# Kernel optimization log

Measured on AMD Instinct MI355X. Metric: run time of the kernel, lower is better.

The kernel has to match this reference:

```python
import jax, jax.numpy as jnp
import numpy as np

H = 16       # num attention heads
DH = 128     # head dim
NEG = -1e9


def setup_inputs() -> dict:
    key = jax.random.key(0)
    ks = jax.random.split(key, 10)
    B, L, HID = 64, 4096, H * DH
    return {
        "hidden_states": jax.random.normal(ks[0], (B, HID), jnp.float32),
        "key_cache": jax.random.normal(ks[1], (B, L, DH), jnp.float32),
        "value_cache": jax.random.normal(ks[2], (B, L, DH), jnp.float32),
        "Wq": jax.random.normal(ks[3], (HID, HID), jnp.float32) * 0.02,
        "bq": jax.random.normal(ks[4], (HID,), jnp.float32) * 0.02,
        "Wkv": jax.random.normal(ks[5], (HID, 2 * DH), jnp.float32) * 0.02,
        "bkv": jax.random.normal(ks[6], (2 * DH,), jnp.float32) * 0.02,
        "Wo": jax.random.normal(ks[7], (HID, HID), jnp.float32) * 0.02,
        "bo": jax.random.normal(ks[8], (HID,), jnp.float32) * 0.02,
        "context_lens": jax.random.randint(ks[9], (B,), 0, L, jnp.int32),
    }


def reference(hidden_states, key_cache, value_cache, Wq, bq, Wkv, bkv, Wo, bo, context_lens):
    B, HID = hidden_states.shape
    L = key_cache.shape[1]
    scale = DH ** -0.5
    # QKV projections (MQA: single KV head)
    q = (hidden_states @ Wq + bq).reshape(B, H, DH)          # [B,H,Dh]
    kv = hidden_states @ Wkv + bkv                            # [B,2*Dh]
    k_new, v_new = kv[:, :DH], kv[:, DH:]                     # [B,Dh] each
    # Attention over paged KV cache (flattened per-sequence view) + current token
    s_cache = jnp.einsum('bhd,bld->bhl', q, key_cache) * scale   # [B,H,L]
    s_self = jnp.einsum('bhd,bd->bh', q, k_new) * scale          # [B,H]
    valid = (jnp.arange(L, dtype=jnp.int32)[None, None, :]
             < context_lens[:, None, None])                      # [B,1,L]
    s_cache = jnp.where(valid, s_cache, NEG)
    scores = jnp.concatenate([s_cache, s_self[..., None]], axis=-1)  # [B,H,L+1]
    p = jax.nn.softmax(scores, axis=-1)
    out = (jnp.einsum('bhl,bld->bhd', p[..., :L], value_cache)
           + p[..., L:] * v_new[:, None, :])                     # [B,H,Dh]
    return out.reshape(B, HID) @ Wo + bo
```

## Files before the change

kernel.cpp:

```cpp
#include <hip/hip_runtime.h>
#include <hip/hip_bf16.h>
#include <math.h>

#define H 16
#define DH 128
#define HID 2048
#define NB 64
#define LCACHE 4096
#define NS 16
#define NKS 16
#define SCALE 0.08838834764831845f

typedef __attribute__((ext_vector_type(8))) short bf16x8;
typedef __attribute__((ext_vector_type(4))) float f32x4;

static __device__ inline unsigned short bfr(float x) {
  union { __hip_bfloat16 b; unsigned short u; } c;
  c.b = __float2bfloat16(x);
  return c.u;
}
static __device__ inline unsigned pkbf(float lo, float hi) {
  return (unsigned)bfr(lo) | ((unsigned)bfr(hi) << 16);
}
union BFU { unsigned u[4]; bf16x8 v; };

__global__ __launch_bounds__(256) void transpose64(const float* __restrict__ A,
                                                   float* __restrict__ At) {
  __shared__ float tile[64 * 65];
  const int k0 = blockIdx.x * 64;
  for (int idx = threadIdx.x; idx < 4096; idx += 256) {
    const int m = idx >> 6, c = idx & 63;
    tile[c * 65 + m] = A[(size_t)m * HID + k0 + c];
  }
  __syncthreads();
  for (int idx = threadIdx.x; idx < 4096; idx += 256) {
    const int c = idx >> 6, m = idx & 63;
    At[(size_t)(k0 + c) * 64 + m] = tile[c * 65 + m];
  }
}

__global__ __launch_bounds__(256, 4) void proj_v2(
    const float* __restrict__ At, const float* __restrict__ W1, const float* __restrict__ W2,
    float* __restrict__ part, int NC1, int NC2) {
  const int NC = NC1 + NC2;
  const int n0 = blockIdx.x * 128;
  const int k0 = blockIdx.y * 128;
  __shared__ float Asub[128 * 68];
  const int t = threadIdx.x;
#pragma unroll
  for (int j = 0; j < 8; ++j) {
    const int f = t * 4 + j * 1024;
    const int k = f >> 6, m = f & 63;
    *(float4*)&Asub[k * 68 + m] = *(const float4*)(At + (size_t)(k0 + k) * 64 + m);
  }
  __syncthreads();
  const int m0 = (t & 15) * 4;
  const int ng = (t >> 4) * 8;
  const float* Wp;
  int ldw, wc;
  if (n0 + ng < NC1) { Wp = W1; ldw = NC1; wc = n0 + ng; }
  else               { Wp = W2; ldw = NC2; wc = n0 + ng - NC1; }
  float acc[4][8];
#pragma unroll
  for (int i = 0; i < 4; ++i)
#pragma unroll
    for (int j = 0; j < 8; ++j) acc[i][j] = 0.f;
#pragma unroll 4
  for (int k = 0; k < 128; ++k) {
    const float4 a4 = *(const float4*)&Asub[k * 68 + m0];
    const float* wrow = Wp + (size_t)(k0 + k) * ldw + wc;
    const float4 w0 = *(const float4*)(wrow);
    const float4 w1 = *(const float4*)(wrow + 4);
    const float av[4] = {a4.x, a4.y, a4.z, a4.w};
    const float wv[8] = {w0.x, w0.y, w0.z, w0.w, w1.x, w1.y, w1.z, w1.w};
#pragma unroll
    for (int i = 0; i < 4; ++i)
#pragma unroll
      for (int j = 0; j < 8; ++j) acc[i][j] = fmaf(av[i], wv[j], acc[i][j]);
  }
#pragma unroll
  for (int i = 0; i < 4; ++i) {
    float4 o1, o2;
    o1.x = acc[i][0]; o1.y = acc[i][1]; o1.z = acc[i][2]; o1.w = acc[i][3];
    o2.x = acc[i][4]; o2.y = acc[i][5]; o2.z = acc[i][6]; o2.w = acc[i][7];
    float* dst = part + ((size_t)blockIdx.y * 64 + m0 + i) * NC + n0 + ng;
    *(float4*)dst = o1;
    *(float4*)(dst + 4) = o2;
  }
}

__global__ __launch_bounds__(256) void proj_combine(
    const float* __restrict__ part, const float* __restrict__ b1, const float* __restrict__ b2,
    float* __restrict__ out1, float* __restrict__ out2, int NC1, int NC2) {
  const int NC = NC1 + NC2;
  const int f = (blockIdx.x * 256 + threadIdx.x) * 4;
  if (f >= 64 * NC) return;
  const int row = f / NC;
  const int c = f - row * NC;
  float4 s = *(const float4*)(part + (size_t)row * NC + c);
#pragma unroll
  for (int sp = 1; sp < NKS; ++sp) {
    const float4 p = *(const float4*)(part + ((size_t)sp * 64 + row) * NC + c);
    s.x += p.x; s.y += p.y; s.z += p.z; s.w += p.w;
  }
  if (c < NC1) {
    const float4 bb = *(const float4*)(b1 + c);
    s.x += bb.x; s.y += bb.y; s.z += bb.z; s.w += bb.w;
    *(float4*)(out1 + (size_t)row * NC1 + c) = s;
  } else {
    const int cc = c - NC1;
    const float4 bb = *(const float4*)(b2 + cc);
    s.x += bb.x; s.y += bb.y; s.z += bb.z; s.w += bb.w;
    *(float4*)(out2 + (size_t)row * NC2 + cc) = s;
  }
}

template <int NSPLIT>
__global__ __launch_bounds__(256, 3) void attn_mfma(
    const float* __restrict__ q_buf, const float* __restrict__ kv_buf,
    const float* __restrict__ key_cache, const float* __restrict__ value_cache,
    const int* __restrict__ lens,
    float* __restrict__ part_out, float* __restrict__ part_m, float* __restrict__ part_l) {
  const int b = blockIdx.y;
  const int sp = blockIdx.x;
  const int ctx = lens[b];
  const int n0 = (ctx * sp) / NSPLIT;
  const int n1 = (ctx * (sp + 1)) / NSPLIT;
  const int cnt = n1 - n0;
  const bool has_self = (sp == NSPLIT - 1);
  const int tot = cnt + (has_self ? 1 : 0);
  const int t = threadIdx.x;
  if (tot == 0) {
    if (t < H) {
      part_m[((size_t)b * NSPLIT + sp) * H + t] = -1e30f;
      part_l[((size_t)b * NSPLIT + sp) * H + t] = 0.f;
    }
    return;
  }
  __shared__ __align__(16) char regA[25024];
  __shared__ __align__(16) char regB[16384];
  __shared__ float red[16 * 17];
  __shared__ float mrow[16];
  __shared__ float selfp[16];

  float* q_s = (float*)regA;
  float* Sm = (float*)(regA + 8448);
  unsigned short* Vt = (unsigned short*)regA;
  char* Kl = regB;
  char* P = regB;

  for (int idx = t; idx < HID; idx += 256)
    q_s[(idx >> 7) * 132 + (idx & 127)] = q_buf[(size_t)b * HID + idx] * SCALE;

  const int lane = t & 63;
  const int wv = t >> 6;
  const int fh = lane & 15;
  const int fg = lane >> 4;
  const int si = t & 63;
  const int sc = t >> 6;
  const int vp = t & 31;
  const int vc = t >> 5;
  const int ntiles = (cnt + 63) >> 6;
  const float* ksrc = key_cache + (size_t)b * LCACHE * DH;
  const float* vsrc = value_cache + (size_t)b * LCACHE * DH;

  float4 kst[8];
  if (ntiles > 0) {
    const int r = min(n0 + si, LCACHE - 1);
    const float* src = ksrc + (size_t)r * DH + sc * 32;
#pragma unroll
    for (int j = 0; j < 8; ++j) kst[j] = *(const float4*)(src + j * 4);
  }
  __syncthreads();

  bf16x8 qf[4];
#pragma unroll
  for (int s = 0; s < 4; ++s) {
    const float4 qa = *(const float4*)&q_s[fh * 132 + s * 32 + fg * 8];
    const float4 qb = *(const float4*)&q_s[fh * 132 + s * 32 + fg * 8 + 4];
    BFU u;
    u.u[0] = pkbf(qa.x, qa.y); u.u[1] = pkbf(qa.z, qa.w);
    u.u[2] = pkbf(qb.x, qb.y); u.u[3] = pkbf(qb.z, qb.w);
    qf[s] = u.v;
  }

  for (int tt = 0; tt < ntiles; ++tt) {
    if (tt > 0) __syncthreads();
#pragma unroll
    for (int s2 = 0; s2 < 4; ++s2) {
      BFU u;
      u.u[0] = pkbf(kst[s2 * 2].x, kst[s2 * 2].y);
      u.u[1] = pkbf(kst[s2 * 2].z, kst[s2 * 2].w);
      u.u[2] = pkbf(kst[s2 * 2 + 1].x, kst[s2 * 2 + 1].y);
      u.u[3] = pkbf(kst[s2 * 2 + 1].z, kst[s2 * 2 + 1].w);
      const int off = si * 256 + ((sc * 64 + s2 * 16) ^ ((si & 7) << 4));
      *(bf16x8*)(Kl + off) = u.v;
    }
    if (tt + 1 < ntiles) {
      const int r = min(n0 + (tt + 1) * 64 + si, LCACHE - 1);
      const float* src = ksrc + (size_t)r * DH + sc * 32;
#pragma unroll
      for (int j = 0; j < 8; ++j) kst[j] = *(const float4*)(src + j * 4);
    }
    __syncthreads();
    f32x4 sacc = {0.f, 0.f, 0.f, 0.f};
    const int rr = wv * 16 + fh;
#pragma unroll
    for (int s = 0; s < 4; ++s) {
      const int off = rr * 256 + ((s * 64 + fg * 16) ^ ((rr & 7) << 4));
      const bf16x8 af = *(const bf16x8*)(Kl + off);
      sacc = __builtin_amdgcn_mfma_f32_16x16x32_bf16(af, qf[s], sacc, 0, 0, 0);
    }
    const int rowl = tt * 64 + wv * 16 + fg * 4;
#pragma unroll
    for (int j = 0; j < 4; ++j) {
      const int rw = rowl + j;
      if (rw < cnt) Sm[fh * 259 + rw] = sacc[j];
    }
  }

  if (ntiles > 0) {
    const int r0g = n0 + 2 * vp;
    const int ra = min(r0g, LCACHE - 1);
    const int rb = min(r0g + 1, LCACHE - 1);
    const float* sa = vsrc + (size_t)ra * DH + vc * 16;
    const float* sb = vsrc + (size_t)rb * DH + vc * 16;
#pragma unroll
    for (int j = 0; j < 4; ++j) {
      kst[j] = *(const float4*)(sa + j * 4);
      kst[4 + j] = *(const float4*)(sb + j * 4);
    }
  }

  if (has_self) {
    if (t < 128) {
      const int h = t >> 3;
      const int seg = t & 7;
      float ps = 0.f;
#pragma unroll
      for (int dd = 0; dd < 16; ++dd)
        ps += q_s[h * 132 + seg * 16 + dd] * kv_buf[(size_t)b * 256 + seg * 16 + dd];
      red[h * 8 + seg] = ps;
    }
    __syncthreads();
    if (t < H) {
      float s = 0.f;
#pragma unroll
      for (int seg = 0; seg < 8; ++seg) s += red[t * 8 + seg];
      Sm[t * 259 + cnt] = s;
    }
  }
  __syncthreads();

  const int hX = t & 15;
  const int g = t >> 4;
  float mloc = -1e30f;
  for (int i = g; i < tot; i += 16) mloc = fmaxf(mloc, Sm[hX * 259 + i]);
  red[hX * 17 + g] = mloc;
  __syncthreads();
  if (t < H) {
    float mx = red[t * 17];
#pragma unroll
    for (int gg = 1; gg < 16; ++gg) mx = fmaxf(mx, red[t * 17 + gg]);
    mrow[t] = mx;
  }
  __syncthreads();
  const float mh = mrow[hX];
  float sloc = 0.f;
  const int ipad = ntiles * 64;
  const int iend = (ipad > tot) ? ipad : tot;
  unsigned short* Pu = (unsigned short*)P;
  for (int i = g; i < iend; i += 16) {
    if (i < cnt) {
      const float e = __expf(Sm[hX * 259 + i] - mh);
      Pu[hX * 264 + i] = bfr(e);
      sloc += e;
    } else {
      if (i < ipad) Pu[hX * 264 + i] = 0;
      if (has_self && i == cnt) {
        const float e = __expf(Sm[hX * 259 + cnt] - mh);
        selfp[hX] = e;
        sloc += e;
      }
    }
  }
  red[hX * 17 + g] = sloc;
  __syncthreads();
  if (t < H) {
    float ls = 0.f;
#pragma unroll
    for (int gg = 0; gg < 16; ++gg) ls += red[t * 17 + gg];
    part_m[((size_t)b * NSPLIT + sp) * H + t] = mrow[t];
    part_l[((size_t)b * NSPLIT + sp) * H + t] = ls;
  }
  __syncthreads();

  f32x4 oacc[2];
  oacc[0] = (f32x4){0.f, 0.f, 0.f, 0.f};
  oacc[1] = (f32x4){0.f, 0.f, 0.f, 0.f};
  unsigned* VtW = (unsigned*)Vt;
  for (int tt = 0; tt < ntiles; ++tt) {
    if (tt > 0) __syncthreads();
#pragma unroll
    for (int j = 0; j < 4; ++j) {
      const float4 a = kst[j];
      const float4 b4 = kst[4 + j];
      const int d = vc * 16 + j * 4;
      VtW[(d + 0) * 44 + vp] = pkbf(a.x, b4.x);
      VtW[(d + 1) * 44 + vp] = pkbf(a.y, b4.y);
      VtW[(d + 2) * 44 + vp] = pkbf(a.z, b4.z);
      VtW[(d + 3) * 44 + vp] = pkbf(a.w, b4.w);
    }
    if (tt + 1 < ntiles) {
      const int r0g = n0 + (tt + 1) * 64 + 2 * vp;
      const int ra = min(r0g, LCACHE - 1);
      const int rb = min(r0g + 1, LCACHE - 1);
      const float* sa = vsrc + (size_t)ra * DH + vc * 16;
      const float* sb = vsrc + (size_t)rb * DH + vc * 16;
#pragma unroll
      for (int j = 0; j < 4; ++j) {
        kst[j] = *(const float4*)(sa + j * 4);
        kst[4 + j] = *(const float4*)(sb + j * 4);
      }
    }
    __syncthreads();
#pragma unroll
    for (int c2 = 0; c2 < 2; ++c2) {
      const bf16x8 pf = *(const bf16x8*)(P + fh * 528 + (tt * 64 + c2 * 32) * 2 + fg * 16);
#pragma unroll
      for (int dt = 0; dt < 2; ++dt) {
        const int d = wv * 32 + dt * 16 + fh;
        const bf16x8 vf = *(const bf16x8*)((char*)Vt + d * 176 + c2 * 64 + fg * 16);
        oacc[dt] = __builtin_amdgcn_mfma_f32_16x16x32_bf16(pf, vf, oacc[dt], 0, 0, 0);
      }
    }
  }

  if (has_self) {
#pragma unroll
    for (int dt = 0; dt < 2; ++dt) {
      const int d = wv * 32 + dt * 16 + fh;
      const float vn = kv_buf[(size_t)b * 256 + 128 + d];
#pragma unroll
      for (int j = 0; j < 4; ++j) oacc[dt][j] = fmaf(selfp[fg * 4 + j], vn, oacc[dt][j]);
    }
  }
  float* po = part_out + (((size_t)b * NSPLIT + sp) * H) * DH;
#pragma unroll
  for (int dt = 0; dt < 2; ++dt) {
    const int d = wv * 32 + dt * 16 + fh;
#pragma unroll
    for (int j = 0; j < 4; ++j) po[(size_t)(fg * 4 + j) * DH + d] = oacc[dt][j];
  }
}

template <int NSPLIT>
__global__ __launch_bounds__(256) void attn_combine(
    const float* __restrict__ part_out, const float* __restrict__ part_m,
    const float* __restrict__ part_l, float* __restrict__ ctx_buf) {
  const int b = blockIdx.x;
  const int dq = blockIdx.y;
  const int t = threadIdx.x;
  const int h = t >> 4;
  const int d = dq * 32 + (t & 15) * 2;
  float M = -1e30f;
#pragma unroll
  for (int sp = 0; sp < NSPLIT; ++sp)
    M = fmaxf(M, part_m[((size_t)b * NSPLIT + sp) * H + h]);
  float L = 0.f, o0 = 0.f, o1 = 0.f;
#pragma unroll
  for (int sp = 0; sp < NSPLIT; ++sp) {
    const float m = part_m[((size_t)b * NSPLIT + sp) * H + h];
    if (m < -1e29f) continue;
    const float w = __expf(m - M);
    L += w * part_l[((size_t)b * NSPLIT + sp) * H + h];
    const float2 a = *(const float2*)(part_out + (((size_t)b * NSPLIT + sp) * H + h) * DH + d);
    o0 = fmaf(w, a.x, o0);
    o1 = fmaf(w, a.y, o1);
  }
  const float inv = 1.f / L;
  float* dst = ctx_buf + (size_t)b * HID + h * DH + d;
  dst[0] = o0 * inv;
  dst[1] = o1 * inv;
}

extern "C" void kernel_launch(void* const* d_in, const int* in_sizes, int n_in,
                              void* d_out, int out_size, void* d_ws, size_t ws_size,
                              hipStream_t stream) {
  const float* hidden      = (const float*)d_in[0];
  const float* key_cache   = (const float*)d_in[1];
  const float* value_cache = (const float*)d_in[2];
  const float* Wq  = (const float*)d_in[3];
  const float* bq  = (const float*)d_in[4];
  const float* Wkv = (const float*)d_in[5];
  const float* bkv = (const float*)d_in[6];
  const float* Wo  = (const float*)d_in[7];
  const float* bo  = (const float*)d_in[8];
  const int*   lens = (const int*)d_in[9];
  float* out = (float*)d_out;

  float* ws = (float*)d_ws;
  float* part1    = ws;
  float* q_buf    = part1 + (size_t)NKS * 64 * 2304;
  float* kv_buf   = q_buf + (size_t)64 * HID;
  float* part_out = kv_buf + (size_t)64 * 256;
  float* part_m   = part_out + (size_t)64 * NS * H * DH;
  float* part_l   = part_m + (size_t)64 * NS * H;
  float* ctx_buf  = part_l + (size_t)64 * NS * H;
  float* part2    = ctx_buf + (size_t)64 * HID;
  float* At       = part2 + (size_t)NKS * 64 * 2048;
  float* ctxT     = At + (size_t)HID * 64;

  transpose64<<<dim3(32), dim3(256), 0, stream>>>(hidden, At);
  proj_v2<<<dim3(18, NKS), dim3(256), 0, stream>>>(At, Wq, Wkv, part1, 2048, 256);
  proj_combine<<<dim3(144), dim3(256), 0, stream>>>(part1, bq, bkv, q_buf, kv_buf, 2048, 256);
  attn_mfma<NS><<<dim3(NS, NB), dim3(256), 0, stream>>>(q_buf, kv_buf, key_cache, value_cache,
                                                        lens, part_out, part_m, part_l);
  attn_combine<NS><<<dim3(NB, 4), dim3(256), 0, stream>>>(part_out, part_m, part_l, ctx_buf);
  transpose64<<<dim3(32), dim3(256), 0, stream>>>(ctx_buf, ctxT);
  proj_v2<<<dim3(16, NKS), dim3(256), 0, stream>>>(ctxT, Wo, Wo, part2, 2048, 0);
  proj_combine<<<dim3(128), dim3(256), 0, stream>>>(part2, bo, bo, out, nullptr, 2048, 0);
}
```

Before: 107.6 us.

## Fuse QK and PV passes into single online-softmax loop, fold transpose into combine

The attention kernel now streams K and V tiles together and keeps a running max and sum (online softmax) per tile. This replaces the earlier pattern of a full score pass into shared memory, a separate softmax pass, and a second PV pass. The scale multiply moves into the projection combine. The attention combine writes the transposed context directly, which removes a separate transpose launch. The cost is more synchronisations per tile and more registers for the dual K/V prefetch, which could reduce occupancy.

```diff
diff --git a/kernel.cpp b/kernel.cpp
--- a/kernel.cpp
+++ b/kernel.cpp
@@ -91,7 +91,7 @@
 
 __global__ __launch_bounds__(256) void proj_combine(
     const float* __restrict__ part, const float* __restrict__ b1, const float* __restrict__ b2,
-    float* __restrict__ out1, float* __restrict__ out2, int NC1, int NC2) {
+    float* __restrict__ out1, float* __restrict__ out2, int NC1, int NC2, float scale1) {
   const int NC = NC1 + NC2;
   const int f = (blockIdx.x * 256 + threadIdx.x) * 4;
   if (f >= 64 * NC) return;
@@ -105,7 +105,8 @@
   }
   if (c < NC1) {
     const float4 bb = *(const float4*)(b1 + c);
-    s.x += bb.x; s.y += bb.y; s.z += bb.z; s.w += bb.w;
+    s.x = (s.x + bb.x) * scale1; s.y = (s.y + bb.y) * scale1;
+    s.z = (s.z + bb.z) * scale1; s.w = (s.w + bb.w) * scale1;
     *(float4*)(out1 + (size_t)row * NC1 + c) = s;
   } else {
     const int cc = c - NC1;
@@ -116,7 +117,7 @@
 }
 
 template <int NSPLIT>
-__global__ __launch_bounds__(256, 3) void attn_mfma(
+__global__ __launch_bounds__(256, 3) void attn_fused(
     const float* __restrict__ q_buf, const float* __restrict__ kv_buf,
     const float* __restrict__ key_cache, const float* __restrict__ value_cache,
     const int* __restrict__ lens,
@@ -128,50 +129,42 @@
   const int n1 = (ctx * (sp + 1)) / NSPLIT;
   const int cnt = n1 - n0;
   const bool has_self = (sp == NSPLIT - 1);
-  const int tot = cnt + (has_self ? 1 : 0);
   const int t = threadIdx.x;
-  if (tot == 0) {
+  if (cnt == 0 && !has_self) {
     if (t < H) {
       part_m[((size_t)b * NSPLIT + sp) * H + t] = -1e30f;
       part_l[((size_t)b * NSPLIT + sp) * H + t] = 0.f;
     }
     return;
   }
-  __shared__ __align__(16) char regA[25024];
-  __shared__ __align__(16) char regB[16384];
-  __shared__ float red[16 * 17];
-  __shared__ float mrow[16];
-  __shared__ float selfp[16];
-
-  float* q_s = (float*)regA;
-  float* Sm = (float*)(regA + 8448);
-  unsigned short* Vt = (unsigned short*)regA;
-  char* Kl = regB;
-  char* P = regB;
+  __shared__ __align__(16) char sV[22528];
+  __shared__ __align__(16) char sK[16384];
+  __shared__ __align__(16) unsigned Pbuf[16 * 36];
+  __shared__ __align__(16) float red1[64];
+  __shared__ __align__(16) float red2[64];
+  __shared__ __align__(16) float mrun[2][16];
+  __shared__ __align__(16) float lrun[2][16];
+  __shared__ __align__(16) float sself[16];
+  __shared__ float sred[128];
+
+  float* q_s = (float*)sV;
+  unsigned* VtW = (unsigned*)sV;
+  unsigned* Kl32 = (unsigned*)sK;
 
   for (int idx = t; idx < HID; idx += 256)
-    q_s[(idx >> 7) * 132 + (idx & 127)] = q_buf[(size_t)b * HID + idx] * SCALE;
+    q_s[(idx >> 7) * 132 + (idx & 127)] = q_buf[(size_t)b * HID + idx];
+  if (t < 16) { mrun[0][t] = -1e30f; lrun[0][t] = 0.f; }
+  __syncthreads();
 
   const int lane = t & 63;
   const int wv = t >> 6;
   const int fh = lane & 15;
   const int fg = lane >> 4;
-  const int si = t & 63;
-  const int sc = t >> 6;
   const int vp = t & 31;
   const int vc = t >> 5;
   const int ntiles = (cnt + 63) >> 6;
   const float* ksrc = key_cache + (size_t)b * LCACHE * DH;
   const float* vsrc = value_cache + (size_t)b * LCACHE * DH;
-
-  float4 kst[8];
-  if (ntiles > 0) {
-    const int r = min(n0 + si, LCACHE - 1);
-    const float* src = ksrc + (size_t)r * DH + sc * 32;
-#pragma unroll
-    for (int j = 0; j < 8; ++j) kst[j] = *(const float4*)(src + j * 4);
-  }
-  __syncthreads();
 
   bf16x8 qf[4];
 #pragma unroll
@@ -183,128 +176,60 @@
     u.u[2] = pkbf(qb.x, qb.y); u.u[3] = pkbf(qb.z, qb.w);
     qf[s] = u.v;
   }
-
-  for (int tt = 0; tt < ntiles; ++tt) {
-    if (tt > 0) __syncthreads();
-#pragma unroll
-    for (int s2 = 0; s2 < 4; ++s2) {
-      BFU u;
-      u.u[0] = pkbf(kst[s2 * 2].x, kst[s2 * 2].y);
-      u.u[1] = pkbf(kst[s2 * 2].z, kst[s2 * 2].w);
-      u.u[2] = pkbf(kst[s2 * 2 + 1].x, kst[s2 * 2 + 1].y);
-      u.u[3] = pkbf(kst[s2 * 2 + 1].z, kst[s2 * 2 + 1].w);
-      const int off = si * 256 + ((sc * 64 + s2 * 16) ^ ((si & 7) << 4));
-      *(bf16x8*)(Kl + off) = u.v;
-    }
-    if (tt + 1 < ntiles) {
-      const int r = min(n0 + (tt + 1) * 64 + si, LCACHE - 1);
-      const float* src = ksrc + (size_t)r * DH + sc * 32;
-#pragma unroll
-      for (int j = 0; j < 8; ++j) kst[j] = *(const float4*)(src + j * 4);
-    }
-    __syncthreads();
-    f32x4 sacc = {0.f, 0.f, 0.f, 0.f};
-    const int rr = wv * 16 + fh;
-#pragma unroll
-    for (int s = 0; s < 4; ++s) {
-      const int off = rr * 256 + ((s * 64 + fg * 16) ^ ((rr & 7) << 4));
-      const bf16x8 af = *(const bf16x8*)(Kl + off);
-      sacc = __builtin_amdgcn_mfma_f32_16x16x32_bf16(af, qf[s], sacc, 0, 0, 0);
-    }
-    const int rowl = tt * 64 + wv * 16 + fg * 4;
+  if (has_self && t < 128) {
+    const int h = t >> 3, seg = t & 7;
+    float ps = 0.f;
+#pragma unroll
+    for (int dd = 0; dd < 16; ++dd)
+      ps += q_s[h * 132 + seg * 16 + dd] * kv_buf[(size_t)b * 256 + seg * 16 + dd];
+    sred[t] = ps;
+  }
+
+  float4 kst[8], vst[8];
+  if (ntiles > 0) {
+    const int tb = n0 * DH;
+#pragma unroll
+    for (int j = 0; j < 8; ++j) {
+      const int off = min(tb + j * 1024 + t * 4, LCACHE * DH - 4);
+      kst[j] = *(const float4*)(ksrc + off);
+    }
+    const int r0 = n0 + 2 * vp;
+    const float* sa = vsrc + (size_t)min(r0, LCACHE - 1) * DH + vc * 16;
+    const float* sb = vsrc + (size_t)min(r0 + 1, LCACHE - 1) * DH + vc * 16;
 #pragma unroll
     for (int j = 0; j < 4; ++j) {
-      const int rw = rowl + j;
-      if (rw < cnt) Sm[fh * 259 + rw] = sacc[j];
-    }
-  }
-
-  if (ntiles > 0) {
-    const int r0g = n0 + 2 * vp;
-    const int ra = min(r0g, LCACHE - 1);
-    const int rb = min(r0g + 1, LCACHE - 1);
-    const float* sa = vsrc + (size_t)ra * DH + vc * 16;
-    const float* sb = vsrc + (size_t)rb * DH + vc * 16;
-#pragma unroll
-    for (int j = 0; j < 4; ++j) {
-      kst[j] = *(const float4*)(sa + j * 4);
-      kst[4 + j] = *(const float4*)(sb + j * 4);
-    }
-  }
-
-  if (has_self) {
-    if (t < 128) {
-      const int h = t >> 3;
-      const int seg = t & 7;
-      float ps = 0.f;
-#pragma unroll
-      for (int dd = 0; dd < 16; ++dd)
-        ps += q_s[h * 132 + seg * 16 + dd] * kv_buf[(size_t)b * 256 + seg * 16 + dd];
-      red[h * 8 + seg] = ps;
-    }
-    __syncthreads();
-    if (t < H) {
-      float s = 0.f;
-#pragma unroll
-      for (int seg = 0; seg < 8; ++seg) s += red[t * 8 + seg];
-      Sm[t * 259 + cnt] = s;
+      vst[j] = *(const float4*)(sa + j * 4);
+      vst[4 + j] = *(const float4*)(sb + j * 4);
     }
   }
   __syncthreads();
 
-  const int hX = t & 15;
-  const int g = t >> 4;
-  float mloc = -1e30f;
-  for (int i = g; i < tot; i += 16) mloc = fmaxf(mloc, Sm[hX * 259 + i]);
-  red[hX * 17 + g] = mloc;
-  __syncthreads();
-  if (t < H) {
-    float mx = red[t * 17];
-#pragma unroll
-    for (int gg = 1; gg < 16; ++gg) mx = fmaxf(mx, red[t * 17 + gg]);
-    mrow[t] = mx;
-  }
-  __syncthreads();
-  const float mh = mrow[hX];
-  float sloc = 0.f;
-  const int ipad = ntiles * 64;
-  const int iend = (ipad > tot) ? ipad : tot;
-  unsigned short* Pu = (unsigned short*)P;
-  for (int i = g; i < iend; i += 16) {
-    if (i < cnt) {
-      const float e = __expf(Sm[hX * 259 + i] - mh);
-      Pu[hX * 264 + i] = bfr(e);
-      sloc += e;
-    } else {
-      if (i < ipad) Pu[hX * 264 + i] = 0;
-      if (has_self && i == cnt) {
-        const float e = __expf(Sm[hX * 259 + cnt] - mh);
-        selfp[hX] = e;
-        sloc += e;
-      }
-    }
-  }
-  red[hX * 17 + g] = sloc;
-  __syncthreads();
-  if (t < H) {
-    float ls = 0.f;
-#pragma unroll
-    for (int gg = 0; gg < 16; ++gg) ls += red[t * 17 + gg];
-    part_m[((size_t)b * NSPLIT + sp) * H + t] = mrow[t];
-    part_l[((size_t)b * NSPLIT + sp) * H + t] = ls;
-  }
-  __syncthreads();
+  if (has_self && t < 16) {
+    float s = 0.f;
+#pragma unroll
+    for (int seg = 0; seg < 8; ++seg) s += sred[t * 8 + seg];
+    sself[t] = s;
+  }
 
   f32x4 oacc[2];
   oacc[0] = (f32x4){0.f, 0.f, 0.f, 0.f};
   oacc[1] = (f32x4){0.f, 0.f, 0.f, 0.f};
-  unsigned* VtW = (unsigned*)Vt;
+  int par = 0;
+
   for (int tt = 0; tt < ntiles; ++tt) {
     if (tt > 0) __syncthreads();
 #pragma unroll
+    for (int j = 0; j < 8; ++j) {
+      const int row = j * 8 + (t >> 5);
+      const int byteo = ((t & 31) * 8) ^ ((row & 7) << 4);
+      const int w0 = row * 64 + (byteo >> 2);
+      Kl32[w0] = pkbf(kst[j].x, kst[j].y);
+      Kl32[w0 + 1] = pkbf(kst[j].z, kst[j].w);
+    }
+#pragma unroll
     for (int j = 0; j < 4; ++j) {
-      const float4 a = kst[j];
-      const float4 b4 = kst[4 + j];
+      const float4 a = vst[j];
+      const float4 b4 = vst[4 + j];
       const int d = vc * 16 + j * 4;
       VtW[(d + 0) * 44 + vp] = pkbf(a.x, b4.x);
       VtW[(d + 1) * 44 + vp] = pkbf(a.y, b4.y);
@@ -312,40 +237,129 @@
       VtW[(d + 3) * 44 + vp] = pkbf(a.w, b4.w);
     }
     if (tt + 1 < ntiles) {
-      const int r0g = n0 + (tt + 1) * 64 + 2 * vp;
-      const int ra = min(r0g, LCACHE - 1);
-      const int rb = min(r0g + 1, LCACHE - 1);
-      const float* sa = vsrc + (size_t)ra * DH + vc * 16;
-      const float* sb = vsrc + (size_t)rb * DH + vc * 16;
+      const int tb = (n0 + (tt + 1) * 64) * DH;
+#pragma unroll
+      for (int j = 0; j < 8; ++j) {
+        const int off = min(tb + j * 1024 + t * 4, LCACHE * DH - 4);
+        kst[j] = *(const float4*)(ksrc + off);
+      }
+      const int r0 = n0 + (tt + 1) * 64 + 2 * vp;
+      const float* sa = vsrc + (size_t)min(r0, LCACHE - 1) * DH + vc * 16;
+      const float* sb = vsrc + (size_t)min(r0 + 1, LCACHE - 1) * DH + vc * 16;
 #pragma unroll
       for (int j = 0; j < 4; ++j) {
-        kst[j] = *(const float4*)(sa + j * 4);
-        kst[4 + j] = *(const float4*)(sb + j * 4);
+        vst[j] = *(const float4*)(sa + j * 4);
+        vst[4 + j] = *(const float4*)(sb + j * 4);
       }
     }
     __syncthreads();
+
+    f32x4 sacc = {0.f, 0.f, 0.f, 0.f};
+    const int rr = wv * 16 + fh;
+#pragma unroll
+    for (int s = 0; s < 4; ++s) {
+      const int off = rr * 256 + ((s * 64 + fg * 16) ^ ((rr & 7) << 4));
+      const bf16x8 af = *(const bf16x8*)(sK + off);
+      sacc = __builtin_amdgcn_mfma_f32_16x16x32_bf16(af, qf[s], sacc, 0, 0, 0);
+    }
+    const int rloc = wv * 16 + fg * 4;
+    const int lim = cnt - tt * 64;
+    float s0 = (rloc + 0 < lim) ? sacc[0] : -1e30f;
+    float s1 = (rloc + 1 < lim) ? sacc[1] : -1e30f;
+    float s2 = (rloc + 2 < lim) ? sacc[2] : -1e30f;
+    float s3 = (rloc + 3 < lim) ? sacc[3] : -1e30f;
+    float ml = fmaxf(fmaxf(s0, s1), fmaxf(s2, s3));
+    ml = fmaxf(ml, __shfl_xor(ml, 16, 64));
+    ml = fmaxf(ml, __shfl_xor(ml, 32, 64));
+    if (fg == 0) red1[wv * 16 + fh] = ml;
+    __syncthreads();
+
+    const float4 r0v = *(const float4*)&red1[0 + fg * 4];
+    const float4 r1v = *(const float4*)&red1[16 + fg * 4];
+    const float4 r2v = *(const float4*)&red1[32 + fg * 4];
+    const float4 r3v = *(const float4*)&red1[48 + fg * 4];
+    float mt[4];
+    mt[0] = fmaxf(fmaxf(r0v.x, r1v.x), fmaxf(r2v.x, r3v.x));
+    mt[1] = fmaxf(fmaxf(r0v.y, r1v.y), fmaxf(r2v.y, r3v.y));
+    mt[2] = fmaxf(fmaxf(r0v.z, r1v.z), fmaxf(r2v.z, r3v.z));
+    mt[3] = fmaxf(fmaxf(r0v.w, r1v.w), fmaxf(r2v.w, r3v.w));
+    float mtf = fmaxf(fmaxf(red1[fh], red1[16 + fh]), fmaxf(red1[32 + fh], red1[48 + fh]));
+    const float4 mp4 = *(const float4*)&mrun[par][fg * 4];
+    const float mpf = mrun[par][fh];
+    const float mnf = fmaxf(mtf, mpf);
+    const float p0 = __expf(s0 - mnf);
+    const float p1 = __expf(s1 - mnf);
+    const float p2 = __expf(s2 - mnf);
+    const float p3 = __expf(s3 - mnf);
+    {
+      const float mpj[4] = {mp4.x, mp4.y, mp4.z, mp4.w};
+#pragma unroll
+      for (int j = 0; j < 4; ++j) {
+        const float mn = fmaxf(mt[j], mpj[j]);
+        const float rf = __expf(mpj[j] - mn);
+        oacc[0][j] *= rf;
+        oacc[1][j] *= rf;
+      }
+    }
+    float sl = p0 + p1 + p2 + p3;
+    sl += __shfl_xor(sl, 16, 64);
+    sl += __shfl_xor(sl, 32, 64);
+    if (fg == 0) red2[wv * 16 + fh] = sl;
+    Pbuf[fh * 36 + wv * 8 + fg * 2] = pkbf(p0, p1);
+    Pbuf[fh * 36 + wv * 8 + fg * 2 + 1] = pkbf(p2, p3);
+    if (t < 16) mrun[par ^ 1][t] = mnf;
+    __syncthreads();
+
+    if (t < 16) {
+      const float lsum = red2[t] + red2[16 + t] + red2[32 + t] + red2[48 + t];
+      const float mpt = mrun[par][t];
+      const float mnt = mrun[par ^ 1][t];
+      lrun[par ^ 1][t] = lrun[par][t] * __expf(mpt - mnt) + lsum;
+    }
 #pragma unroll
     for (int c2 = 0; c2 < 2; ++c2) {
-      const bf16x8 pf = *(const bf16x8*)(P + fh * 528 + (tt * 64 + c2 * 32) * 2 + fg * 16);
+      const bf16x8 pf = *(const bf16x8*)&Pbuf[fh * 36 + c2 * 16 + fg * 4];
 #pragma unroll
       for (int dt = 0; dt < 2; ++dt) {
         const int d = wv * 32 + dt * 16 + fh;
-        const bf16x8 vf = *(const bf16x8*)((char*)Vt + d * 176 + c2 * 64 + fg * 16);
+        const bf16x8 vf = *(const bf16x8*)&VtW[d * 44 + c2 * 16 + fg * 4];
         oacc[dt] = __builtin_amdgcn_mfma_f32_16x16x32_bf16(pf, vf, oacc[dt], 0, 0, 0);
       }
     }
-  }
-
+    par ^= 1;
+  }
+  __syncthreads();
+
+  const int parF = par;
   if (has_self) {
-#pragma unroll
-    for (int dt = 0; dt < 2; ++dt) {
-      const int d = wv * 32 + dt * 16 + fh;
-      const float vn = kv_buf[(size_t)b * 256 + 128 + d];
-#pragma unroll
-      for (int j = 0; j < 4; ++j) oacc[dt][j] = fmaf(selfp[fg * 4 + j], vn, oacc[dt][j]);
-    }
-  }
-  float* po = part_out + (((size_t)b * NSPLIT + sp) * H) * DH;
+    const float4 mp4 = *(const float4*)&mrun[parF][fg * 4];
+    const float4 ss4 = *(const float4*)&sself[fg * 4];
+    const float vn0 = kv_buf[(size_t)b * 256 + 128 + wv * 32 + fh];
+    const float vn1 = kv_buf[(size_t)b * 256 + 128 + wv * 32 + 16 + fh];
+    const float mpj[4] = {mp4.x, mp4.y, mp4.z, mp4.w};
+    const float ssj[4] = {ss4.x, ss4.y, ss4.z, ss4.w};
+#pragma unroll
+    for (int j = 0; j < 4; ++j) {
+      const float mn = fmaxf(mpj[j], ssj[j]);
+      const float rf = __expf(mpj[j] - mn);
+      const float ps = __expf(ssj[j] - mn);
+      oacc[0][j] = oacc[0][j] * rf + ps * vn0;
+      oacc[1][j] = oacc[1][j] * rf + ps * vn1;
+    }
+    if (t < 16) {
+      const float mp = mrun[parF][t], ss = sself[t];
+      const float mn = fmaxf(mp, ss);
+      part_m[((size_t)b * NSPLIT + sp) * H + t] = mn;
+      part_l[((size_t)b * NSPLIT + sp) * H + t] =
+          lrun[parF][t] * __expf(mp - mn) + __expf(ss - mn);
+    }
+  } else {
+    if (t < 16) {
+      part_m[((size_t)b * NSPLIT + sp) * H + t] = mrun[parF][t];
+      part_l[((size_t)b * NSPLIT + sp) * H + t] = lrun[parF][t];
+    }
+  }
+  float* po = part_out + ((size_t)b * NSPLIT + sp) * H * DH;
 #pragma unroll
   for (int dt = 0; dt < 2; ++dt) {
     const int d = wv * 32 + dt * 16 + fh;
@@ -354,34 +368,38 @@
   }
 }
 
-template <int NSPLIT>
-__global__ __launch_bounds__(256) void attn_combine(
+__global__ __launch_bounds__(256) void attn_combineT(
     const float* __restrict__ part_out, const float* __restrict__ part_m,
-    const float* __restrict__ part_l, float* __restrict__ ctx_buf) {
-  const int b = blockIdx.x;
-  const int dq = blockIdx.y;
-  const int t = threadIdx.x;
-  const int h = t >> 4;
-  const int d = dq * 32 + (t & 15) * 2;
+    const float* __restrict__ part_l, float* __restrict__ ctxT) {
+  const int h = blockIdx.x;
+  const int d0 = blockIdx.y * 32 + (threadIdx.x >> 6) * 8;
+  const int b = threadIdx.x & 63;
   float M = -1e30f;
 #pragma unroll
-  for (int sp = 0; sp < NSPLIT; ++sp)
-    M = fmaxf(M, part_m[((size_t)b * NSPLIT + sp) * H + h]);
-  float L = 0.f, o0 = 0.f, o1 = 0.f;
-#pragma unroll
-  for (int sp = 0; sp < NSPLIT; ++sp) {
-    const float m = part_m[((size_t)b * NSPLIT + sp) * H + h];
+  for (int sp = 0; sp < NS; ++sp)
+    M = fmaxf(M, part_m[((size_t)b * NS + sp) * H + h]);
+  float L = 0.f;
+  float o[8];
+#pragma unroll
+  for (int i = 0; i < 8; ++i) o[i] = 0.f;
+#pragma unroll
+  for (int sp = 0; sp < NS; ++sp) {
+    const float m = part_m[((size_t)b * NS + sp) * H + h];
     if (m < -1e29f) continue;
     const float w = __expf(m - M);
-    L += w * part_l[((size_t)b * NSPLIT + sp) * H + h];
-    const float2 a = *(const float2*)(part_out + (((size_t)b * NSPLIT + sp) * H + h) * DH + d);
-    o0 = fmaf(w, a.x, o0);
-    o1 = fmaf(w, a.y, o1);
+    L += w * part_l[((size_t)b * NS + sp) * H + h];
+    const float* src = part_out + (((size_t)b * NS + sp) * H + h) * DH + d0;
+    const float4 a = *(const float4*)src;
+    const float4 c = *(const float4*)(src + 4);
+    o[0] = fmaf(w, a.x, o[0]); o[1] = fmaf(w, a.y, o[1]);
+    o[2] = fmaf(w, a.z, o[2]); o[3] = fmaf(w, a.w, o[3]);
+    o[4] = fmaf(w, c.x, o[4]); o[5] = fmaf(w, c.y, o[5]);
+    o[6] = fmaf(w, c.z, o[6]); o[7] = fmaf(w, c.w, o[7]);
   }
   const float inv = 1.f / L;
-  float* dst = ctx_buf + (size_t)b * HID + h * DH + d;
-  dst[0] = o0 * inv;
-  dst[1] = o1 * inv;
+#pragma unroll
+  for (int i = 0; i < 8; ++i)
+    ctxT[(size_t)(h * DH + d0 + i) * 64 + b] = o[i] * inv;
 }
 
 extern "C" void kernel_launch(void* const* d_in, const int* in_sizes, int n_in,
@@ -406,18 +424,16 @@
   float* part_out = kv_buf + (size_t)64 * 256;
   float* part_m   = part_out + (size_t)64 * NS * H * DH;
   float* part_l   = part_m + (size_t)64 * NS * H;
-  float* ctx_buf  = part_l + (size_t)64 * NS * H;
-  float* part2    = ctx_buf + (size_t)64 * HID;
+  float* ctxT     = part_l + (size_t)64 * NS * H;
+  float* part2    = ctxT + (size_t)HID * 64;
   float* At       = part2 + (size_t)NKS * 64 * 2048;
-  float* ctxT     = At + (size_t)HID * 64;
 
   transpose64<<<dim3(32), dim3(256), 0, stream>>>(hidden, At);
   proj_v2<<<dim3(18, NKS), dim3(256), 0, stream>>>(At, Wq, Wkv, part1, 2048, 256);
-  proj_combine<<<dim3(144), dim3(256), 0, stream>>>(part1, bq, bkv, q_buf, kv_buf, 2048, 256);
-  attn_mfma<NS><<<dim3(NS, NB), dim3(256), 0, stream>>>(q_buf, kv_buf, key_cache, value_cache,
-                                                        lens, part_out, part_m, part_l);
-  attn_combine<NS><<<dim3(NB, 4), dim3(256), 0, stream>>>(part_out, part_m, part_l, ctx_buf);
-  transpose64<<<dim3(32), dim3(256), 0, stream>>>(ctx_buf, ctxT);
+  proj_combine<<<dim3(144), dim3(256), 0, stream>>>(part1, bq, bkv, q_buf, kv_buf, 2048, 256, SCALE);
+  attn_fused<NS><<<dim3(NS, NB), dim3(256), 0, stream>>>(q_buf, kv_buf, key_cache, value_cache,
+                                                         lens, part_out, part_m, part_l);
+  attn_combineT<<<dim3(H, 4), dim3(256), 0, stream>>>(part_out, part_m, part_l, ctxT);
   proj_v2<<<dim3(16, NKS), dim3(256), 0, stream>>>(ctxT, Wo, Wo, part2, 2048, 0);
-  proj_combine<<<dim3(128), dim3(256), 0, stream>>>(part2, bo, bo, out, nullptr, 2048, 0);
-}
+  proj_combine<<<dim3(128), dim3(256), 0, stream>>>(part2, bo, bo, out, nullptr, 2048, 0, 1.0f);
+}
```

Result: faster. 101.3 us (-5.8%).
